# Optimization experiments

Hardware: AMD Instinct MI355X
Metric: run time of the kernel (lower is better)

## Reference

```python
import jax, jax.numpy as jnp
import numpy as np

EPS = 1e-5          # denominator epsilon from module
PROJ_EPS = 4e-3     # geoopt float32 projection epsilon
MIN_NORM = 1e-15


def _sabs(x):
    return jnp.abs(x) + MIN_NORM


def _sign(x):
    # geoopt sign: sign(0) == 1
    return jnp.sign(jnp.sign(x) + 0.5)


def _clamp_abs(x, eps):
    return _sign(x) * jnp.maximum(jnp.abs(x), eps)


def _lambda_x(x, k):
    # conformal factor 2 / (1 + k ||x||^2)
    return 2.0 / jnp.maximum(1.0 + k * jnp.sum(x * x, axis=-1, keepdims=True), MIN_NORM)


def _parallel_transport0back(x, v, k):
    # transport v at x back to the origin: v / (1 + k ||x||^2)
    return v / jnp.maximum(1.0 + k * jnp.sum(x * x, axis=-1, keepdims=True), MIN_NORM)


def _artan_k(x, k):
    sk = jnp.sqrt(_sabs(k))
    hyp = jnp.arctanh(jnp.minimum(sk * x, 1.0 - 1e-7)) / sk   # k < 0
    sph = jnp.arctan(sk * x) / sk                              # k > 0
    return jnp.where(k < 0, hyp, sph)


def _tan_k(x, k):
    sk = jnp.sqrt(_sabs(k))
    return jnp.where(k < 0, jnp.tanh(sk * x) / sk, jnp.tan(sk * x) / sk)


def _project(x, k):
    maxnorm = (1.0 - PROJ_EPS) / jnp.sqrt(_sabs(k))
    maxnorm = jnp.where(k < 0, maxnorm, 1e15)
    norm = jnp.maximum(jnp.linalg.norm(x, axis=-1, keepdims=True), MIN_NORM)
    return jnp.where(norm > maxnorm, x / norm * maxnorm, x)


def _mobius_scalar_mul(r, x, k):
    xn = jnp.maximum(jnp.linalg.norm(x, axis=-1, keepdims=True), MIN_NORM)
    return _tan_k(r * _artan_k(xn, k), k) * (x / xn)


def setup_inputs() -> dict:
    key = jax.random.key(0)
    kQ, kK, kV = jax.random.split(key, 3)
    B, H, N, D = 4, 16, 4096, 64
    Q = jax.random.normal(kQ, (B, H, N, D), dtype=jnp.float32)
    K = jax.random.normal(kK, (B, H, N, D), dtype=jnp.float32)
    # V holds points on the Poincare ball: scale so ||V|| < 1
    V = 0.05 * jax.random.normal(kV, (B, H, N, D), dtype=jnp.float32)
    mask = jnp.ones((N,), dtype=jnp.float32)
    c = jnp.array([-1.0], dtype=jnp.float32)  # hyperbolic curvature (geoopt k-convention)
    return {"Q": Q, "K": K, "V": V, "mask": mask, "c": c}


def reference(Q, K, V, mask, c):
    H = Q.shape[-3]
    curv = jnp.broadcast_to(c.reshape(-1), (H,)) if c.shape[0] == 1 else c
    curv = curv[:, None, None]  # [H,1,1] broadcasts over [B,H,N,D]

    x = V
    v1 = _parallel_transport0back(x, Q, curv)
    v2 = _parallel_transport0back(x, K, curv)
    gamma = _lambda_x(x, curv)                     # [B,H,N,1]
    denom = _clamp_abs(gamma - 1.0, 1e-10)
    m = mask[None, :, None]                        # [1,N,1]
    x = gamma / denom * x * m
    v1 = jax.nn.elu(v1) + 1.0
    v2 = denom * (jax.nn.elu(v2) + 1.0) * m

    v2_sum = jnp.sum(v2, axis=-2)                  # [B,H,D]
    D = jnp.einsum('...nd,...d->...n', v1, v2_sum)
    D_inv = 1.0 / jnp.where(D == 0, EPS, D)
    context = jnp.einsum('...nd,...ne->...de', v2, x)   # [B,H,D,D]
    X = jnp.einsum('...de,...nd,...n->...ne', context, v1, D_inv)

    X = _project(X, curv)
    X = _mobius_scalar_mul(0.5, X, curv)
    X = _project(X, curv)
    return X
```

## Files before the change

kernel.cpp:

```cpp
#include <hip/hip_runtime.h>
#include <math.h>

#define EPS_C      1e-05f
#define PROJ_EPS_C 0.004f
#define MIN_NORM_C 1e-15f

#define NTOK   4096
#define DH     64
#define TILE   64
#define CHUNK2 128
#define NCHUNK2 (NTOK / CHUNK2)
#define PADROW 68

#define FMA4(ACC, S, B)                      \
    ACC.x = fmaf((S), (B).x, ACC.x);         \
    ACC.y = fmaf((S), (B).y, ACC.y);         \
    ACC.z = fmaf((S), (B).z, ACC.z);         \
    ACC.w = fmaf((S), (B).w, ACC.w);

__device__ __forceinline__ float elup(float z) {
    return z > 0.f ? z + 1.f : __expf(z);
}

__global__ __launch_bounds__(256, 4) void glin_phase1(
    const float* __restrict__ Kk, const float* __restrict__ Vv,
    const float* __restrict__ mask, const float* __restrict__ cc,
    int csize, int H, int chunk_toks, int BH,
    float* __restrict__ pt_out,
    float* __restrict__ part_v2, float* __restrict__ part_ctx)
{
    __shared__ __align__(16) float v2s[TILE][PADROW];
    __shared__ __align__(16) float xss[TILE][PADROW];

    const int bh    = blockIdx.x;
    const int chunk = blockIdx.y;
    const int h     = bh % H;
    const float k   = cc[(csize == 1) ? 0 : h];

    const float* Kp = Kk + (size_t)bh * NTOK * DH;
    const float* Vp = Vv + (size_t)bh * NTOK * DH;
    float* ptp      = pt_out + (size_t)bh * NTOK;

    const int tid = threadIdx.x;
    const int ty  = tid >> 4;
    const int tx  = tid & 15;

    float4 acc0 = {0.f, 0.f, 0.f, 0.f};
    float4 acc1 = {0.f, 0.f, 0.f, 0.f};
    float4 acc2 = {0.f, 0.f, 0.f, 0.f};
    float4 acc3 = {0.f, 0.f, 0.f, 0.f};
    float4 v2acc = {0.f, 0.f, 0.f, 0.f};

    const int tbase = chunk * chunk_toks;
    for (int tt = 0; tt < chunk_toks; tt += TILE) {
#pragma unroll
        for (int p = 0; p < 4; ++p) {
            int f   = tid + p * 256;
            int row = f >> 4;
            int c4  = f & 15;
            int gtok = tbase + tt + row;
            float4 v4 = *(const float4*)(Vp + (size_t)gtok * DH + c4 * 4);
            float4 k4 = *(const float4*)(Kp + (size_t)gtok * DH + c4 * 4);
            float ss = v4.x * v4.x + v4.y * v4.y + v4.z * v4.z + v4.w * v4.w;
            ss += __shfl_xor(ss, 1);
            ss += __shfl_xor(ss, 2);
            ss += __shfl_xor(ss, 4);
            ss += __shfl_xor(ss, 8);
            float dpt   = fmaxf(1.f + k * ss, MIN_NORM_C);
            float pt    = 1.f / dpt;
            float gamma = 2.f * pt;
            float gm1   = gamma - 1.f;
            float sg    = (gm1 < 0.f) ? -1.f : 1.f;
            float denomG = sg * fmaxf(fabsf(gm1), 1e-10f);
            float m     = mask[gtok];
            float xsc   = gamma / denomG * m;
            float a2    = denomG * m;
            if (c4 == 0) ptp[gtok] = pt;
            float4 xs4;
            xs4.x = v4.x * xsc; xs4.y = v4.y * xsc;
            xs4.z = v4.z * xsc; xs4.w = v4.w * xsc;
            float4 w4;
            w4.x = a2 * elup(k4.x * pt);
            w4.y = a2 * elup(k4.y * pt);
            w4.z = a2 * elup(k4.z * pt);
            w4.w = a2 * elup(k4.w * pt);
            *(float4*)&xss[row][c4 * 4] = xs4;
            *(float4*)&v2s[row][c4 * 4] = w4;
        }
        __syncthreads();
#pragma unroll 8
        for (int t = 0; t < TILE; ++t) {
            float4 a = *(const float4*)&v2s[t][ty * 4];
            float4 b = *(const float4*)&xss[t][tx * 4];
            v2acc.x += a.x; v2acc.y += a.y; v2acc.z += a.z; v2acc.w += a.w;
            FMA4(acc0, a.x, b);
            FMA4(acc1, a.y, b);
            FMA4(acc2, a.z, b);
            FMA4(acc3, a.w, b);
        }
        __syncthreads();
    }

    float* pc = part_ctx + ((size_t)chunk * BH + bh) * (DH * DH);
    *(float4*)&pc[(ty * 4 + 0) * DH + tx * 4] = acc0;
    *(float4*)&pc[(ty * 4 + 1) * DH + tx * 4] = acc1;
    *(float4*)&pc[(ty * 4 + 2) * DH + tx * 4] = acc2;
    *(float4*)&pc[(ty * 4 + 3) * DH + tx * 4] = acc3;
    if (tx == 0) {
        float* pv = part_v2 + ((size_t)chunk * BH + bh) * DH;
        *(float4*)&pv[ty * 4] = v2acc;
    }
}

__global__ __launch_bounds__(256) void glin_reduce(
    const float* __restrict__ part_ctx, const float* __restrict__ part_v2,
    int P, int BH,
    float* __restrict__ ctx_out, float* __restrict__ v2sum_out)
{
    const int bh  = blockIdx.x;
    const int q   = blockIdx.y;
    const int tid = threadIdx.x;
    const int base = q * 1024 + tid;

    float s0 = 0.f, s1 = 0.f, s2 = 0.f, s3 = 0.f;
    for (int c = 0; c < P; ++c) {
        const float* p = part_ctx + ((size_t)c * BH + bh) * (DH * DH);
        s0 += p[base];
        s1 += p[base + 256];
        s2 += p[base + 512];
        s3 += p[base + 768];
    }
    float* co = ctx_out + (size_t)bh * DH * DH;
    co[base] = s0; co[base + 256] = s1; co[base + 512] = s2; co[base + 768] = s3;

    if (q == 0 && tid < DH) {
        float s = 0.f;
        for (int c = 0; c < P; ++c)
            s += part_v2[((size_t)c * BH + bh) * DH + tid];
        v2sum_out[(size_t)bh * DH + tid] = s;
    }
}

__device__ __forceinline__ void epilogue_store(
    float4 x, float dv, float k, float sk, float maxnorm,
    float* __restrict__ outp, int gtok, int tx)
{
    x.x *= dv; x.y *= dv; x.z *= dv; x.w *= dv;
    float n2 = x.x * x.x + x.y * x.y + x.z * x.z + x.w * x.w;
    n2 += __shfl_xor(n2, 1);
    n2 += __shfl_xor(n2, 2);
    n2 += __shfl_xor(n2, 4);
    n2 += __shfl_xor(n2, 8);
    float n  = fmaxf(sqrtf(n2), MIN_NORM_C);
    float scale = 1.f;
    float n1 = n;
    if (n > maxnorm) { scale = maxnorm / n; n1 = maxnorm; }
    float xn = fmaxf(n1, MIN_NORM_C);
    float s2;
    if (k < 0.f) {
        float t = fminf(sk * xn, 1.f - 1e-7f);
        s2 = 1.f / (1.f + sqrtf(fmaxf(1.f - t * t, 0.f)));
    } else {
        float t = sk * xn;
        s2 = 1.f / (1.f + sqrtf(1.f + t * t));
    }
    scale *= s2;
    float nrm2 = fmaxf(n1 * s2, MIN_NORM_C);
    if (nrm2 > maxnorm) scale *= maxnorm / nrm2;
    float4 o;
    o.x = x.x * scale; o.y = x.y * scale;
    o.z = x.z * scale; o.w = x.w * scale;
    *(float4*)(outp + (size_t)gtok * DH + tx * 4) = o;
}

__global__ __launch_bounds__(256, 4) void glin_phase2(
    const float* __restrict__ Qq, const float* __restrict__ cc,
    int csize, int H,
    const float* __restrict__ pt_in, const float* __restrict__ v2sum_in,
    const float* __restrict__ ctx_in, float* __restrict__ out)
{
    __shared__ __align__(16) float ctxs[DH][PADROW];
    __shared__ __align__(16) float v1s[TILE][PADROW];
    __shared__ __align__(16) float v2sum[DH];
    __shared__ float dinv[TILE];
    __shared__ __align__(16) float ptl[CHUNK2];

    const int bh    = blockIdx.x;
    const int chunk = blockIdx.y;
    const int h     = bh % H;
    const float k   = cc[(csize == 1) ? 0 : h];
    const float sk  = sqrtf(fabsf(k) + MIN_NORM_C);
    const float maxnorm = (k < 0.f) ? (1.f - PROJ_EPS_C) / sk : 1e15f;

    const int tid = threadIdx.x;
    const int ty  = tid >> 4;
    const int tx  = tid & 15;

    const float* Qp = Qq + (size_t)bh * NTOK * DH;
    float* outp     = out + (size_t)bh * NTOK * DH;

#pragma unroll
    for (int p = 0; p < 4; ++p) {
        int f = tid + p * 256;
        int d = f >> 4, c4 = f & 15;
        float4 v = *(const float4*)(ctx_in + (size_t)bh * DH * DH + d * DH + c4 * 4);
        *(float4*)&ctxs[d][c4 * 4] = v;
    }
    if (tid < 16) {
        float4 v = *(const float4*)(v2sum_in + (size_t)bh * DH + tid * 4);
        *(float4*)&v2sum[tid * 4] = v;
    }
    if (tid < CHUNK2 / 4) {
        float4 v = *(const float4*)(pt_in + (size_t)bh * NTOK + chunk * CHUNK2 + tid * 4);
        *(float4*)&ptl[tid * 4] = v;
    }
    __syncthreads();

    const int tbase = chunk * CHUNK2;
    for (int tt = 0; tt < CHUNK2; tt += TILE) {
#pragma unroll
        for (int p = 0; p < 4; ++p) {
            int f   = tid + p * 256;
            int row = f >> 4;
            int c4  = f & 15;
            int gtok = tbase + tt + row;
            float4 q4 = *(const float4*)(Qp + (size_t)gtok * DH + c4 * 4);
            float ptv = ptl[tt + row];
            float4 v1;
            v1.x = elup(q4.x * ptv);
            v1.y = elup(q4.y * ptv);
            v1.z = elup(q4.z * ptv);
            v1.w = elup(q4.w * ptv);
            float4 vs = *(const float4*)&v2sum[c4 * 4];
            float dp = v1.x * vs.x + v1.y * vs.y + v1.z * vs.z + v1.w * vs.w;
            dp += __shfl_xor(dp, 1);
            dp += __shfl_xor(dp, 2);
            dp += __shfl_xor(dp, 4);
            dp += __shfl_xor(dp, 8);
            if (c4 == 0) {
                float Dv = (dp == 0.f) ? EPS_C : dp;
                dinv[row] = 1.f / Dv;
            }
            *(float4*)&v1s[row][c4 * 4] = v1;
        }
        __syncthreads();
        float4 acc0 = {0.f, 0.f, 0.f, 0.f};
        float4 acc1 = {0.f, 0.f, 0.f, 0.f};
        float4 acc2 = {0.f, 0.f, 0.f, 0.f};
        float4 acc3 = {0.f, 0.f, 0.f, 0.f};
#pragma unroll 8
        for (int db = 0; db < DH / 4; ++db) {
            float4 b0 = *(const float4*)&ctxs[db * 4 + 0][tx * 4];
            float4 b1 = *(const float4*)&ctxs[db * 4 + 1][tx * 4];
            float4 b2 = *(const float4*)&ctxs[db * 4 + 2][tx * 4];
            float4 b3 = *(const float4*)&ctxs[db * 4 + 3][tx * 4];
            float4 a0 = *(const float4*)&v1s[ty * 4 + 0][db * 4];
            FMA4(acc0, a0.x, b0); FMA4(acc0, a0.y, b1);
            FMA4(acc0, a0.z, b2); FMA4(acc0, a0.w, b3);
            float4 a1 = *(const float4*)&v1s[ty * 4 + 1][db * 4];
            FMA4(acc1, a1.x, b0); FMA4(acc1, a1.y, b1);
            FMA4(acc1, a1.z, b2); FMA4(acc1, a1.w, b3);
            float4 a2 = *(const float4*)&v1s[ty * 4 + 2][db * 4];
            FMA4(acc2, a2.x, b0); FMA4(acc2, a2.y, b1);
            FMA4(acc2, a2.z, b2); FMA4(acc2, a2.w, b3);
            float4 a3 = *(const float4*)&v1s[ty * 4 + 3][db * 4];
            FMA4(acc3, a3.x, b0); FMA4(acc3, a3.y, b1);
            FMA4(acc3, a3.z, b2); FMA4(acc3, a3.w, b3);
        }
        epilogue_store(acc0, dinv[ty * 4 + 0], k, sk, maxnorm, outp, tbase + tt + ty * 4 + 0, tx);
        epilogue_store(acc1, dinv[ty * 4 + 1], k, sk, maxnorm, outp, tbase + tt + ty * 4 + 1, tx);
        epilogue_store(acc2, dinv[ty * 4 + 2], k, sk, maxnorm, outp, tbase + tt + ty * 4 + 2, tx);
        epilogue_store(acc3, dinv[ty * 4 + 3], k, sk, maxnorm, outp, tbase + tt + ty * 4 + 3, tx);
        __syncthreads();
    }
}

extern "C" void kernel_launch(void* const* d_in, const int* in_sizes, int n_in,
                              void* d_out, int out_size, void* d_ws, size_t ws_size,
                              hipStream_t stream)
{
    const float* Q    = (const float*)d_in[0];
    const float* K    = (const float*)d_in[1];
    const float* V    = (const float*)d_in[2];
    const float* mask = (const float*)d_in[3];
    const float* c    = (const float*)d_in[4];
    const int csize   = in_sizes[4];
    const int BH      = in_sizes[0] / (NTOK * DH);
    const int H       = 16;
    float* out        = (float*)d_out;

    int P = 16;
    while (P > 1) {
        size_t need = ((size_t)BH * NTOK
                     + (size_t)BH * DH
                     + (size_t)BH * DH * DH
                     + (size_t)P * BH * DH
                     + (size_t)P * BH * DH * DH)
                     * sizeof(float);
        if (need <= ws_size) break;
        P >>= 1;
    }
    const int chunk_toks = NTOK / P;

    float* pt       = (float*)d_ws;
    float* v2sum    = pt + (size_t)BH * NTOK;
    float* ctx      = v2sum + (size_t)BH * DH;
    float* part_v2  = ctx + (size_t)BH * DH * DH;
    float* part_ctx = part_v2 + (size_t)P * BH * DH;

    dim3 g1(BH, P);
    glin_phase1<<<g1, 256, 0, stream>>>(K, V, mask, c, csize, H, chunk_toks, BH,
                                        pt, part_v2, part_ctx);
    dim3 gr(BH, 4);
    glin_reduce<<<gr, 256, 0, stream>>>(part_ctx, part_v2, P, BH, ctx, v2sum);
    dim3 g2(BH, NCHUNK2);
    glin_phase2<<<g2, 256, 0, stream>>>(Q, c, csize, H, pt, v2sum, ctx, out);
}
```

Before: 276.9 us.

## Give each wavefront its own token slice and reduce context across warps

Phase1 now splits each block's token chunk across its four wavefronts. Each wave stages a 16-token sub-tile in private shared memory and computes a full 64x64 outer-product accumulator (8x8 per lane) with no block-wide barriers in the main loop. The four per-wave partial contexts are combined through shared memory at the end. The reduce kernel is also split into more blocks with one element per thread, for more parallelism. In exchange, register pressure rises sharply (128 accumulator floats) and an intra-block reduction is added, which may lower occupancy under the launch bound of 4 blocks.

```diff
diff --git a/kernel.cpp b/kernel.cpp
--- a/kernel.cpp
+++ b/kernel.cpp
@@ -11,12 +11,17 @@
 #define CHUNK2 128
 #define NCHUNK2 (NTOK / CHUNK2)
 #define PADROW 68
+#define SUB    16
 
 #define FMA4(ACC, S, B)                      \
     ACC.x = fmaf((S), (B).x, ACC.x);         \
     ACC.y = fmaf((S), (B).y, ACC.y);         \
     ACC.z = fmaf((S), (B).z, ACC.z);         \
     ACC.w = fmaf((S), (B).w, ACC.w);
+
+#define ADD4(ACC, B)                         \
+    ACC.x += (B).x; ACC.y += (B).y;          \
+    ACC.z += (B).z; ACC.w += (B).w;
 
 __device__ __forceinline__ float elup(float z) {
     return z > 0.f ? z + 1.f : __expf(z);
@@ -29,8 +34,8 @@
     float* __restrict__ pt_out,
     float* __restrict__ part_v2, float* __restrict__ part_ctx)
 {
-    __shared__ __align__(16) float v2s[TILE][PADROW];
-    __shared__ __align__(16) float xss[TILE][PADROW];
+    __shared__ __align__(16) float stg[4][2][SUB][PADROW];
+    __shared__ __align__(16) float v2red[4][DH];
 
     const int bh    = blockIdx.x;
     const int chunk = blockIdx.y;
@@ -41,24 +46,36 @@
     const float* Vp = Vv + (size_t)bh * NTOK * DH;
     float* ptp      = pt_out + (size_t)bh * NTOK;
 
-    const int tid = threadIdx.x;
-    const int ty  = tid >> 4;
-    const int tx  = tid & 15;
-
-    float4 acc0 = {0.f, 0.f, 0.f, 0.f};
-    float4 acc1 = {0.f, 0.f, 0.f, 0.f};
-    float4 acc2 = {0.f, 0.f, 0.f, 0.f};
-    float4 acc3 = {0.f, 0.f, 0.f, 0.f};
-    float4 v2acc = {0.f, 0.f, 0.f, 0.f};
-
-    const int tbase = chunk * chunk_toks;
-    for (int tt = 0; tt < chunk_toks; tt += TILE) {
+    const int tid  = threadIdx.x;
+    const int w    = tid >> 6;
+    const int lane = tid & 63;
+    const int r    = lane >> 3;
+    const int cg   = lane & 7;
+    const int srow = lane >> 4;
+    const int c4   = lane & 15;
+
+    float (*v2w)[PADROW] = stg[w][0];
+    float (*xsw)[PADROW] = stg[w][1];
+
+    float4 acc[8][2];
+#pragma unroll
+    for (int i = 0; i < 8; ++i) {
+        acc[i][0] = make_float4(0.f, 0.f, 0.f, 0.f);
+        acc[i][1] = make_float4(0.f, 0.f, 0.f, 0.f);
+    }
+    float4 va0 = make_float4(0.f, 0.f, 0.f, 0.f);
+    float4 va1 = make_float4(0.f, 0.f, 0.f, 0.f);
+
+    const int wtok  = chunk_toks >> 2;
+    const int wbase = chunk * chunk_toks + w * wtok;
+
+    for (int s = 0; s < wtok; s += SUB) {
+        asm volatile("s_waitcnt lgkmcnt(0)" ::: "memory");
+        __builtin_amdgcn_sched_barrier(0);
 #pragma unroll
         for (int p = 0; p < 4; ++p) {
-            int f   = tid + p * 256;
-            int row = f >> 4;
-            int c4  = f & 15;
-            int gtok = tbase + tt + row;
+            const int row  = p * 4 + srow;
+            const int gtok = wbase + s + row;
             float4 v4 = *(const float4*)(Vp + (size_t)gtok * DH + c4 * 4);
             float4 k4 = *(const float4*)(Kp + (size_t)gtok * DH + c4 * 4);
             float ss = v4.x * v4.x + v4.y * v4.y + v4.z * v4.z + v4.w * v4.w;
@@ -76,39 +93,97 @@
             float xsc   = gamma / denomG * m;
             float a2    = denomG * m;
             if (c4 == 0) ptp[gtok] = pt;
-            float4 xs4;
-            xs4.x = v4.x * xsc; xs4.y = v4.y * xsc;
-            xs4.z = v4.z * xsc; xs4.w = v4.w * xsc;
-            float4 w4;
-            w4.x = a2 * elup(k4.x * pt);
-            w4.y = a2 * elup(k4.y * pt);
-            w4.z = a2 * elup(k4.z * pt);
-            w4.w = a2 * elup(k4.w * pt);
-            *(float4*)&xss[row][c4 * 4] = xs4;
-            *(float4*)&v2s[row][c4 * 4] = w4;
-        }
-        __syncthreads();
-#pragma unroll 8
-        for (int t = 0; t < TILE; ++t) {
-            float4 a = *(const float4*)&v2s[t][ty * 4];
-            float4 b = *(const float4*)&xss[t][tx * 4];
-            v2acc.x += a.x; v2acc.y += a.y; v2acc.z += a.z; v2acc.w += a.w;
-            FMA4(acc0, a.x, b);
-            FMA4(acc1, a.y, b);
-            FMA4(acc2, a.z, b);
-            FMA4(acc3, a.w, b);
-        }
-        __syncthreads();
-    }
-
-    float* pc = part_ctx + ((size_t)chunk * BH + bh) * (DH * DH);
-    *(float4*)&pc[(ty * 4 + 0) * DH + tx * 4] = acc0;
-    *(float4*)&pc[(ty * 4 + 1) * DH + tx * 4] = acc1;
-    *(float4*)&pc[(ty * 4 + 2) * DH + tx * 4] = acc2;
-    *(float4*)&pc[(ty * 4 + 3) * DH + tx * 4] = acc3;
-    if (tx == 0) {
-        float* pv = part_v2 + ((size_t)chunk * BH + bh) * DH;
-        *(float4*)&pv[ty * 4] = v2acc;
+            v4.x *= xsc; v4.y *= xsc; v4.z *= xsc; v4.w *= xsc;
+            k4.x = a2 * elup(k4.x * pt);
+            k4.y = a2 * elup(k4.y * pt);
+            k4.z = a2 * elup(k4.z * pt);
+            k4.w = a2 * elup(k4.w * pt);
+            *(float4*)&xsw[row][c4 * 4] = v4;
+            *(float4*)&v2w[row][c4 * 4] = k4;
+        }
+        asm volatile("s_waitcnt lgkmcnt(0)" ::: "memory");
+        __builtin_amdgcn_sched_barrier(0);
+#pragma unroll 4
+        for (int t = 0; t < SUB; ++t) {
+            const float4 a0 = *(const float4*)&v2w[t][r * 8];
+            const float4 a1 = *(const float4*)&v2w[t][r * 8 + 4];
+            const float4 b0 = *(const float4*)&xsw[t][cg * 8];
+            const float4 b1 = *(const float4*)&xsw[t][cg * 8 + 4];
+            ADD4(va0, a0);
+            ADD4(va1, a1);
+            FMA4(acc[0][0], a0.x, b0); FMA4(acc[0][1], a0.x, b1);
+            FMA4(acc[1][0], a0.y, b0); FMA4(acc[1][1], a0.y, b1);
+            FMA4(acc[2][0], a0.z, b0); FMA4(acc[2][1], a0.z, b1);
+            FMA4(acc[3][0], a0.w, b0); FMA4(acc[3][1], a0.w, b1);
+            FMA4(acc[4][0], a1.x, b0); FMA4(acc[4][1], a1.x, b1);
+            FMA4(acc[5][0], a1.y, b0); FMA4(acc[5][1], a1.y, b1);
+            FMA4(acc[6][0], a1.z, b0); FMA4(acc[6][1], a1.z, b1);
+            FMA4(acc[7][0], a1.w, b0); FMA4(acc[7][1], a1.w, b1);
+        }
+    }
+
+    if (cg == 0) {
+        *(float4*)&v2red[w][r * 8]     = va0;
+        *(float4*)&v2red[w][r * 8 + 4] = va1;
+    }
+    __syncthreads();
+
+    float* red   = &stg[0][0][0][0];
+    const int eo = cg * 8;
+    if (w == 1) {
+#pragma unroll
+        for (int i = 0; i < 8; ++i) {
+            *(float4*)&red[(r * 8 + i) * DH + eo]     = acc[i][0];
+            *(float4*)&red[(r * 8 + i) * DH + eo + 4] = acc[i][1];
+        }
+    } else if (w == 3) {
+#pragma unroll
+        for (int i = 0; i < 8; ++i) {
+            *(float4*)&red[4096 + (r * 8 + i) * DH + eo]     = acc[i][0];
+            *(float4*)&red[4096 + (r * 8 + i) * DH + eo + 4] = acc[i][1];
+        }
+    }
+    __syncthreads();
+    if (w == 0) {
+#pragma unroll
+        for (int i = 0; i < 8; ++i) {
+            float4 t0 = *(const float4*)&red[(r * 8 + i) * DH + eo];
+            float4 t1 = *(const float4*)&red[(r * 8 + i) * DH + eo + 4];
+            ADD4(acc[i][0], t0);
+            ADD4(acc[i][1], t1);
+        }
+    } else if (w == 2) {
+#pragma unroll
+        for (int i = 0; i < 8; ++i) {
+            float4 t0 = *(const float4*)&red[4096 + (r * 8 + i) * DH + eo];
+            float4 t1 = *(const float4*)&red[4096 + (r * 8 + i) * DH + eo + 4];
+            ADD4(acc[i][0], t0);
+            ADD4(acc[i][1], t1);
+        }
+    } else if (w == 1) {
+        float sv = v2red[0][lane] + v2red[1][lane] + v2red[2][lane] + v2red[3][lane];
+        part_v2[((size_t)chunk * BH + bh) * DH + lane] = sv;
+    }
+    __syncthreads();
+    if (w == 2) {
+#pragma unroll
+        for (int i = 0; i < 8; ++i) {
+            *(float4*)&red[(r * 8 + i) * DH + eo]     = acc[i][0];
+            *(float4*)&red[(r * 8 + i) * DH + eo + 4] = acc[i][1];
+        }
+    }
+    __syncthreads();
+    if (w == 0) {
+        float* pc = part_ctx + ((size_t)chunk * BH + bh) * (DH * DH);
+#pragma unroll
+        for (int i = 0; i < 8; ++i) {
+            float4 t0 = *(const float4*)&red[(r * 8 + i) * DH + eo];
+            float4 t1 = *(const float4*)&red[(r * 8 + i) * DH + eo + 4];
+            ADD4(acc[i][0], t0);
+            ADD4(acc[i][1], t1);
+            *(float4*)&pc[(r * 8 + i) * DH + eo]     = acc[i][0];
+            *(float4*)&pc[(r * 8 + i) * DH + eo + 4] = acc[i][1];
+        }
     }
 }
 
@@ -117,21 +192,15 @@
     int P, int BH,
     float* __restrict__ ctx_out, float* __restrict__ v2sum_out)
 {
-    const int bh  = blockIdx.x;
-    const int q   = blockIdx.y;
-    const int tid = threadIdx.x;
-    const int base = q * 1024 + tid;
-
-    float s0 = 0.f, s1 = 0.f, s2 = 0.f, s3 = 0.f;
-    for (int c = 0; c < P; ++c) {
-        const float* p = part_ctx + ((size_t)c * BH + bh) * (DH * DH);
-        s0 += p[base];
-        s1 += p[base + 256];
-        s2 += p[base + 512];
-        s3 += p[base + 768];
-    }
-    float* co = ctx_out + (size_t)bh * DH * DH;
-    co[base] = s0; co[base + 256] = s1; co[base + 512] = s2; co[base + 768] = s3;
+    const int bh   = blockIdx.x;
+    const int q    = blockIdx.y;
+    const int tid  = threadIdx.x;
+    const int base = q * 256 + tid;
+
+    float s0 = 0.f;
+    for (int c = 0; c < P; ++c)
+        s0 += part_ctx[((size_t)c * BH + bh) * (DH * DH) + base];
+    ctx_out[(size_t)bh * DH * DH + base] = s0;
 
     if (q == 0 && tid < DH) {
         float s = 0.f;
@@ -311,7 +380,7 @@
     dim3 g1(BH, P);
     glin_phase1<<<g1, 256, 0, stream>>>(K, V, mask, c, csize, H, chunk_toks, BH,
                                         pt, part_v2, part_ctx);
-    dim3 gr(BH, 4);
+    dim3 gr(BH, 16);
     glin_reduce<<<gr, 256, 0, stream>>>(part_ctx, part_v2, P, BH, ctx, v2sum);
     dim3 g2(BH, NCHUNK2);
     glin_phase2<<<g2, 256, 0, stream>>>(Q, c, csize, H, pt, v2sum, ctx, out);
```

Measured after the change: 275.3 us. About the same (-0.6%).
